# Kernel optimization log

Measured on AMD Instinct MI355X. Metric: run time of the kernel, lower is better.

## Reference

```python
import math
import jax, jax.numpy as jnp
import numpy as np

D_MODEL = 1024
D_STATE = 16
D_CONV = 4
EXPAND = 2
N_MOD = 2
D_INNER = EXPAND * D_MODEL
DT_RANK = math.ceil(D_MODEL / 16)
B_SZ = 2
SEQLEN = 2048


def setup_inputs() -> dict:
    key = jax.random.key(0)
    ks = jax.random.split(key, 10)
    hidden_states = jax.random.normal(ks[0], (B_SZ, SEQLEN, D_MODEL), jnp.float32)
    modality_ids = jax.random.randint(ks[1], (B_SZ, SEQLEN), 0, N_MOD).astype(jnp.int32)
    W_in = jax.random.normal(ks[2], (N_MOD, 2 * D_INNER, D_MODEL), jnp.float32) * (D_MODEL ** -0.5)
    conv_w = jax.random.normal(ks[3], (D_INNER, D_CONV), jnp.float32) * (D_CONV ** -0.5)
    conv_b = jnp.zeros((D_INNER,), jnp.float32)
    W_x = jax.random.normal(ks[4], (N_MOD, DT_RANK + 2 * D_STATE, D_INNER), jnp.float32) * (D_INNER ** -0.5)
    dt_init_std = DT_RANK ** -0.5
    W_dt = jax.random.uniform(ks[5], (N_MOD, D_INNER, DT_RANK), jnp.float32, -dt_init_std, dt_init_std)
    # dt bias init: inverse-softplus of dt ~ LogUniform(dt_min, dt_max), per Mamba
    dt = jnp.exp(jax.random.uniform(ks[6], (N_MOD, D_INNER), jnp.float32)
                 * (math.log(0.1) - math.log(0.001)) + math.log(0.001))
    dt = jnp.maximum(dt, 1e-4)
    b_dt = dt + jnp.log(-jnp.expm1(-dt))
    A_log = jnp.log(jnp.broadcast_to(jnp.arange(1, D_STATE + 1, dtype=jnp.float32), (D_INNER, D_STATE)))
    D = jnp.ones((D_INNER,), jnp.float32)
    W_out = jax.random.normal(ks[7], (N_MOD, D_MODEL, D_INNER), jnp.float32) * (D_INNER ** -0.5)
    return dict(hidden_states=hidden_states, modality_ids=modality_ids, W_in=W_in,
                conv_w=conv_w, conv_b=conv_b, W_x=W_x, W_dt=W_dt, b_dt=b_dt,
                A_log=A_log, D=D, W_out=W_out)


def _expert_apply(x, W, ids):
    # x: [T, d_in], W: [E, d_out, d_in], ids: [T] -> per-token expert output [T, d_out]
    all_out = jnp.einsum('td,eod->teo', x, W)
    return jnp.take_along_axis(all_out, ids[:, None, None], axis=1)[:, 0, :]


def _forward(hidden_states, modality_ids, W_in, conv_w, conv_b, W_x, W_dt, b_dt, A_log, D, W_out):
    Bsz, L, d_model = hidden_states.shape
    d_inner, d_state = A_log.shape
    dt_rank = W_dt.shape[2]
    d_conv = conv_w.shape[1]
    ids = modality_ids.reshape(-1)  # [T]

    # per-modality in_proj dispatch/combine
    xz = _expert_apply(hidden_states.reshape(-1, d_model), W_in, ids)  # [T, 2*d_inner]
    xz = xz.reshape(Bsz, L, 2 * d_inner).transpose(0, 2, 1)            # [B, 2*d_inner, L]
    x, z = jnp.split(xz, 2, axis=1)                                    # [B, d_inner, L] each

    # causal depthwise conv1d (pad left d_conv-1, truncate to L) + SiLU
    xp = jnp.pad(x, ((0, 0), (0, 0), (d_conv - 1, 0)))
    xc = conv_b[None, :, None]
    for k in range(d_conv):
        xc = xc + conv_w[None, :, k:k + 1] * xp[:, :, k:k + L]
    x = jax.nn.silu(xc)

    # per-modality x_proj -> (dt, B, C)
    xt = x.transpose(0, 2, 1).reshape(-1, d_inner)                     # [T, d_inner]
    x_dbl = _expert_apply(xt, W_x, ids)
    dt, Bm, Cm = jnp.split(x_dbl, [dt_rank, dt_rank + d_state], axis=-1)

    # per-modality dt_proj (with bias), then softplus (delta_softplus=True)
    dt = _expert_apply(dt, W_dt, ids) + b_dt[ids]                      # [T, d_inner]
    dt = jax.nn.softplus(dt)

    A = -jnp.exp(A_log)                                                # [d_inner, d_state]

    # selective scan over sequence (time-major)
    dts = dt.reshape(Bsz, L, d_inner).transpose(1, 0, 2)               # [L, B, d_inner]
    Bms = Bm.reshape(Bsz, L, d_state).transpose(1, 0, 2)               # [L, B, d_state]
    Cms = Cm.reshape(Bsz, L, d_state).transpose(1, 0, 2)               # [L, B, d_state]
    xs = x.transpose(2, 0, 1)                                          # [L, B, d_inner]

    def step(state, inp):
        x_t, dt_t, B_t, C_t = inp
        dA = jnp.exp(dt_t[..., None] * A)                              # [B, d_inner, d_state]
        state = state * dA + (dt_t * x_t)[..., None] * B_t[:, None, :]
        y_t = jnp.einsum('bdn,bn->bd', state, C_t)
        return state, y_t

    init = jnp.zeros((Bsz, d_inner, d_state), jnp.float32)
    _, ys = jax.lax.scan(step, init, (xs, dts, Bms, Cms))              # ys: [L, B, d_inner]

    y = ys.transpose(1, 0, 2)                                          # [B, L, d_inner]
    y = y + x.transpose(0, 2, 1) * D[None, None, :]                    # skip D*u
    y = y * jax.nn.silu(z.transpose(0, 2, 1))                          # z gate

    # per-modality out_proj
    out = _expert_apply(y.reshape(-1, d_inner), W_out, ids)
    return out.reshape(Bsz, L, d_model)


def reference(hidden_states, modality_ids, W_in, conv_w, conv_b, W_x, W_dt, b_dt, A_log, D, W_out):
    return _forward(hidden_states, modality_ids, W_in, conv_w, conv_b, W_x, W_dt, b_dt, A_log, D, W_out)
```

## Files before the change

### kernel.cpp

```cpp
#include <hip/hip_runtime.h>
#include <hip/hip_bf16.h>
#include <math.h>

#define B_SZ 2
#define SEQLEN 2048
#define D_MODEL 1024
#define D_INNER 2048
#define D_STATE 16
#define D_CONV 4
#define DT_RANK 64
#define NTOK (B_SZ * SEQLEN)
#define XDBL 96
#define NC 32
#define LC 64
#define PADTOT (17 * 256)

typedef float f32x4 __attribute__((ext_vector_type(4)));
typedef unsigned int u32x4 __attribute__((ext_vector_type(4)));
typedef __hip_bfloat16 bf16;

__device__ __forceinline__ float siluf(float v) { return v / (1.f + __expf(-v)); }
__device__ __forceinline__ float softplusf(float v) {
  return (v > 20.f) ? v : __logf(1.f + __expf(v));
}

__device__ __forceinline__ void mfma_bf16(f32x4& acc, u32x4 a, u32x4 b) {
  asm volatile("v_mfma_f32_16x16x32_bf16 %0, %1, %2, %0" : "+v"(acc) : "v"(a), "v"(b));
}

__device__ __forceinline__ void gload16(const bf16* g, bf16* l) {
  __builtin_amdgcn_global_load_lds(
      (const __attribute__((address_space(1))) unsigned int*)g,
      (__attribute__((address_space(3))) unsigned int*)l, 16, 0, 0);
}

__global__ __launch_bounds__(1024) void k_perm(const int* __restrict__ ids, int* __restrict__ perm) {
  __shared__ int sc[1024];
  const int tid = threadIdx.x;
  int loc[4];
  int cnt = 0;
#pragma unroll
  for (int q = 0; q < 4; q++) {
    loc[q] = ids[tid * 4 + q];
    cnt += (loc[q] == 0);
  }
  sc[tid] = cnt;
  __syncthreads();
  for (int off = 1; off < 1024; off <<= 1) {
    int v = sc[tid];
    int u = (tid >= off) ? sc[tid - off] : 0;
    __syncthreads();
    sc[tid] = v + u;
    __syncthreads();
  }
  const int N0 = sc[1023];
  const int m0 = (N0 + 255) & ~255;
  const int N1 = NTOK - N0;
  for (int idx = tid; idx < PADTOT; idx += 1024)
    if ((idx >= N0 && idx < m0) || idx >= m0 + N1) perm[idx] = -1;
  int zb = sc[tid] - cnt;
#pragma unroll
  for (int q = 0; q < 4; q++) {
    int t = tid * 4 + q;
    if (loc[q] == 0) { perm[zb] = t; zb++; }
    else             { perm[m0 + (t - zb)] = t; }
  }
}

#define CVT_H   (NTOK * D_MODEL)
#define CVT_WIN (2 * 2 * D_INNER * D_MODEL)
#define CVT_WX  (2 * XDBL * D_INNER)
#define CVT_WDT (2 * D_INNER * DT_RANK)
#define CVT_WO  (2 * D_MODEL * D_INNER)
#define CVT_TOT (CVT_H + CVT_WIN + CVT_WX + CVT_WDT + CVT_WO)
__global__ __launch_bounds__(256) void k_cvtall(const float* __restrict__ h,
                                                const float* __restrict__ Win,
                                                const float* __restrict__ Wx,
                                                const float* __restrict__ Wdt,
                                                const float* __restrict__ Wout,
                                                bf16* __restrict__ hB, bf16* __restrict__ WinB,
                                                bf16* __restrict__ WxB, bf16* __restrict__ WdtB,
                                                bf16* __restrict__ WoB) {
  size_t i = ((size_t)blockIdx.x * 256 + threadIdx.x) * 8;
  const float* src; bf16* dst; size_t off;
  if (i < CVT_H)                          { src = h;    dst = hB;   off = i; }
  else if (i < CVT_H + CVT_WIN)           { src = Win;  dst = WinB; off = i - CVT_H; }
  else if (i < CVT_H + CVT_WIN + CVT_WX)  { src = Wx;   dst = WxB;  off = i - CVT_H - CVT_WIN; }
  else if (i < CVT_TOT - CVT_WO)          { src = Wdt;  dst = WdtB; off = i - CVT_H - CVT_WIN - CVT_WX; }
  else                                    { src = Wout; dst = WoB;  off = i - (CVT_TOT - CVT_WO); }
  float4 f0 = *(const float4*)&src[off];
  float4 f1 = *(const float4*)&src[off + 4];
  __align__(16) bf16 tmp[8];
  tmp[0] = __float2bfloat16(f0.x); tmp[1] = __float2bfloat16(f0.y);
  tmp[2] = __float2bfloat16(f0.z); tmp[3] = __float2bfloat16(f0.w);
  tmp[4] = __float2bfloat16(f1.x); tmp[5] = __float2bfloat16(f1.y);
  tmp[6] = __float2bfloat16(f1.z); tmp[7] = __float2bfloat16(f1.w);
  *(u32x4*)&dst[off] = *(const u32x4*)tmp;
}

template <int KDIM, int NW, int KSPLIT, int EPI>
__device__ __forceinline__ void gemmP_body(const bf16* __restrict__ actB,
                                           const int* __restrict__ perm,
                                           const int* __restrict__ ids,
                                           const bf16* __restrict__ WB,
                                           bf16* __restrict__ outx,
                                           bf16* __restrict__ outz,
                                           float* __restrict__ out0) {
  constexpr int KLEN = KDIM / KSPLIT;
  constexpr int NT = KLEN / 64;
  constexpr int NCOL = (EPI == 1) ? (D_MODEL / 128) : 0;
  __shared__ bf16 As[3][256 * 64];
  __shared__ bf16 Ws[3][128 * 64];
  const int tid = threadIdx.x;

  const int gx = gridDim.x;
  const int nwg = gx * gridDim.y;
  const int fid = blockIdx.y * gx + blockIdx.x;
  const int q8 = nwg >> 3;
  const int swz = (fid & 7) * q8 + (fid >> 3);
  const int bx = swz % gx, by = swz / gx;
  const int ot = (KSPLIT > 1) ? (bx % NCOL) * 128 : bx * 128;
  const int kz = (KSPLIT > 1) ? bx / NCOL : 0;
  const int kbase = kz * KLEN;
  const int tt = by * 256;

  const int lane = tid & 63, w = tid >> 6;
  const int wr = w >> 1, wc = w & 1;
  const int lr = lane & 15, lg = lane >> 4;

  const int t00 = perm[tt];
  const int eu = (t00 >= 0) ? ids[t00] : 0;
  const size_t wexp = (size_t)eu * NW * KDIM;

  const int kswz = ((lane & 7) ^ ((lane >> 3) & 7)) * 8;
  size_t aBase[4]; int aLds[4];
  size_t bBase[2]; int bLds[2];
#pragma unroll
  for (int v = 0; v < 4; v++) {
    const int row = w * 32 + v * 8 + (lane >> 3);
    int ta = perm[tt + row]; if (ta < 0) ta = 0;
    aBase[v] = (size_t)ta * KDIM + kswz;
    aLds[v] = (w * 32 + v * 8) * 64;
  }
#pragma unroll
  for (int v = 0; v < 2; v++) {
    const int row = w * 16 + v * 8 + (lane >> 3);
    bBase[v] = wexp + (size_t)(ot + row) * KDIM + kswz;
    bLds[v] = (w * 16 + v * 8) * 64;
  }

  f32x4 acc[4][4];
#pragma unroll
  for (int i = 0; i < 4; i++)
#pragma unroll
    for (int j = 0; j < 4; j++) acc[i][j] = (f32x4){0.f, 0.f, 0.f, 0.f};

#pragma unroll
  for (int kt = 0; kt < 2; kt++) {
    const int k0 = kbase + kt * 64;
    gload16(&actB[aBase[0] + k0], &As[kt][aLds[0]]);
    gload16(&actB[aBase[1] + k0], &As[kt][aLds[1]]);
    gload16(&actB[aBase[2] + k0], &As[kt][aLds[2]]);
    gload16(&actB[aBase[3] + k0], &As[kt][aLds[3]]);
    gload16(&WB[bBase[0] + k0], &Ws[kt][bLds[0]]);
    gload16(&WB[bBase[1] + k0], &Ws[kt][bLds[1]]);
  }

  int bR = 0, bS = 2;
  for (int kt = 0; kt < NT; ++kt) {
    const int kp = kbase + (kt + 2) * 64;
    const bool st = (kt + 2 < NT);
    if (st) {
      gload16(&actB[aBase[0] + kp], &As[bS][aLds[0]]);
      gload16(&actB[aBase[1] + kp], &As[bS][aLds[1]]);
      gload16(&WB[bBase[0] + kp], &Ws[bS][bLds[0]]);
    }
    if (kt < NT - 2)       asm volatile("s_waitcnt vmcnt(9)" ::: "memory");
    else if (kt == NT - 2) asm volatile("s_waitcnt vmcnt(6)" ::: "memory");
    else                   asm volatile("s_waitcnt vmcnt(0)" ::: "memory");
    asm volatile("s_barrier" ::: "memory");

    const bf16* Ab = As[bR];
    const bf16* Wb = Ws[bR];
    u32x4 a[4][2], b0[2][2];
#pragma unroll
    for (int f = 0; f < 4; f++)
#pragma unroll
      for (int s = 0; s < 2; s++) {
        const int row = wr * 64 + f * 16 + lr;
        a[f][s] = *(const u32x4*)&Ab[row * 64 + ((s * 4 + lg) ^ (row & 7)) * 8];
      }
#pragma unroll
    for (int j = 0; j < 2; j++)
#pragma unroll
      for (int s = 0; s < 2; s++) {
        const int row = wc * 64 + j * 16 + lr;
        b0[j][s] = *(const u32x4*)&Wb[row * 64 + ((s * 4 + lg) ^ (row & 7)) * 8];
      }
    __builtin_amdgcn_s_setprio(1);
#pragma unroll
    for (int f = 0; f < 4; f++)
#pragma unroll
      for (int j = 0; j < 2; j++) {
        mfma_bf16(acc[f][j], a[f][0], b0[j][0]);
        mfma_bf16(acc[f][j], a[f][1], b0[j][1]);
      }
    __builtin_amdgcn_s_setprio(0);

    if (st) {
      gload16(&actB[aBase[2] + kp], &As[bS][aLds[2]]);
      gload16(&actB[aBase[3] + kp], &As[bS][aLds[3]]);
      gload16(&WB[bBase[1] + kp], &Ws[bS][bLds[1]]);
    }
    u32x4 b1[2][2];
#pragma unroll
    for (int j = 0; j < 2; j++)
#pragma unroll
      for (int s = 0; s < 2; s++) {
        const int row = wc * 64 + (2 + j) * 16 + lr;
        b1[j][s] = *(const u32x4*)&Wb[row * 64 + ((s * 4 + lg) ^ (row & 7)) * 8];
      }
    __builtin_amdgcn_s_setprio(1);
#pragma unroll
    for (int f = 0; f < 4; f++)
#pragma unroll
      for (int j = 0; j < 2; j++) {
        mfma_bf16(acc[f][2 + j], a[f][0], b1[j][0]);
        mfma_bf16(acc[f][2 + j], a[f][1], b1[j][1]);
      }
    __builtin_amdgcn_s_setprio(0);
    asm volatile("s_waitcnt lgkmcnt(0)" ::: "memory");
    asm volatile("s_barrier" ::: "memory");
    bR = (bR == 2) ? 0 : bR + 1;
    bS = (bS == 2) ? 0 : bS + 1;
  }

#pragma unroll
  for (int i = 0; i < 4; i++) {
#pragma unroll
    for (int r = 0; r < 4; r++) {
      const int m = wr * 64 + i * 16 + lg * 4 + r;
      const int t = perm[tt + m];
      if (t < 0) continue;
#pragma unroll
      for (int j = 0; j < 4; j++) {
        const int col = ot + wc * 64 + j * 16 + lr;
        const float v = acc[i][j][r];
        if (EPI == 0) {
          const bf16 vb = __float2bfloat16(v);
          if (col < D_INNER) outx[(size_t)t * D_INNER + col] = vb;
          else outz[(size_t)t * D_INNER + (col - D_INNER)] = vb;
        } else {
          out0[((size_t)kz * NTOK + t) * D_MODEL + col] = v;
        }
      }
    }
  }
}

__global__ __launch_bounds__(512) void k_inproj(const bf16* actB, const int* perm, const int* ids,
                                                const bf16* WB, bf16* outx, bf16* outz) {
  gemmP_body<D_MODEL, 2 * D_INNER, 1, 0>(actB, perm, ids, WB, outx, outz, nullptr);
}
__global__ __launch_bounds__(512) void k_outproj(const bf16* actB, const int* perm, const int* ids,
                                                 const bf16* WB, float* out0) {
  gemmP_body<D_INNER, D_MODEL, 2, 1>(actB, perm, ids, WB, nullptr, nullptr, out0);
}

__global__ __launch_bounds__(256) void k_xdblg(const bf16* __restrict__ actB,
                                               const int* __restrict__ perm,
                                               const int* __restrict__ ids,
                                               const bf16* __restrict__ WB,
                                               float* __restrict__ out0) {
  constexpr int KDIM = D_INNER, NW = XDBL, LDO = XDBL, KSPLIT = 8;
  constexpr int KLEN = KDIM / KSPLIT;
  __shared__ bf16 As[128 * 64];
  __shared__ bf16 Ws[128 * 64];
  __shared__ int permL[128];
  const int tid = threadIdx.x;
  const int bx = blockIdx.x, by = blockIdx.y;

  const int ot = 0;
  const int kz = bx;
  const int kbase = kz * KLEN;
  const int tt = by * 128;

  if (tid < 128) permL[tid] = perm[tt + tid];

  const int lane = tid & 63, w = tid >> 6;
  const int wr = w >> 1, wc = w & 1;
  const int lr = lane & 15, lg = lane >> 4;

  const int t00 = perm[tt];
  const int eu = (t00 >= 0) ? ids[t00] : 0;
  const size_t wexp = (size_t)eu * NW * KDIM;

  const int srow = w * 32 + (lane >> 3);
  const int scol = (lane & 7) * 8;
  size_t abase[4], bbase[4];
  int ldsoff[4];
#pragma unroll
  for (int v = 0; v < 4; v++) {
    const int row = srow + v * 8;
    int ta = perm[tt + row];
    if (ta < 0) ta = 0;
    abase[v] = (size_t)ta * KDIM + scol;
    int orow = ot + row;
    orow = (orow < NW) ? orow : (NW - 1);
    bbase[v] = wexp + (size_t)orow * KDIM + scol;
    ldsoff[v] = (w * 32 + v * 8) * 64;
  }

  f32x4 acc[4][4];
#pragma unroll
  for (int i = 0; i < 4; i++)
#pragma unroll
    for (int j = 0; j < 4; j++) acc[i][j] = (f32x4){0.f, 0.f, 0.f, 0.f};

  for (int k0 = kbase; k0 < kbase + KLEN; k0 += 64) {
#pragma unroll
    for (int v = 0; v < 4; v++) {
      gload16(&actB[abase[v] + k0], &As[ldsoff[v]]);
      gload16(&WB[bbase[v] + k0], &Ws[ldsoff[v]]);
    }
    __syncthreads();
#pragma unroll
    for (int ks = 0; ks < 64; ks += 32) {
      u32x4 a[4], b[4];
#pragma unroll
      for (int f = 0; f < 4; f++)
        a[f] = *(const u32x4*)&As[(wr * 64 + f * 16 + lr) * 64 + ks + lg * 8];
#pragma unroll
      for (int f = 0; f < 4; f++)
        b[f] = *(const u32x4*)&Ws[(wc * 64 + f * 16 + lr) * 64 + ks + lg * 8];
#pragma unroll
      for (int i = 0; i < 4; i++)
#pragma unroll
        for (int j = 0; j < 4; j++) mfma_bf16(acc[i][j], a[i], b[j]);
    }
    __syncthreads();
  }

#pragma unroll
  for (int i = 0; i < 4; i++) {
#pragma unroll
    for (int r = 0; r < 4; r++) {
      const int m = wr * 64 + i * 16 + lg * 4 + r;
      const int t = permL[m];
      if (t < 0) continue;
#pragma unroll
      for (int j = 0; j < 4; j++) {
        const int col = ot + wc * 64 + j * 16 + lr;
        if (col < NW) out0[((size_t)kz * NTOK + t) * LDO + col] = acc[i][j][r];
      }
    }
  }
}

__global__ __launch_bounds__(256, 4) void k_dtv(const float* __restrict__ xdbl,
                                                const int* __restrict__ perm,
                                                const int* __restrict__ ids,
                                                const float* __restrict__ Wdt,
                                                const float* __restrict__ bdt,
                                                bf16* __restrict__ dtB) {
  __shared__ float Xs[64][65];
  __shared__ float Ws[64][65];
  __shared__ int permL[64];
  const int tid = threadIdx.x;
  const int tt = blockIdx.y * 64;
  const int cb = blockIdx.x * 64;
  if (tid < 64) permL[tid] = perm[tt + tid];
  const int t0 = perm[tt];
  const int e = (t0 >= 0) ? ids[t0] : 0;
  {
    const int r = tid >> 2, q = (tid & 3) * 16;
    int ta = perm[tt + r];
    if (ta < 0) ta = 0;
    const float* xsrc = &xdbl[(size_t)ta * XDBL + q];
    const float* wsrc = &Wdt[((size_t)e * D_INNER + cb + r) * DT_RANK + q];
#pragma unroll
    for (int u = 0; u < 4; u++) {
      float4 xv = *(const float4*)&xsrc[u * 4];
      float4 wv = *(const float4*)&wsrc[u * 4];
      *(float4*)&Xs[r][q + u * 4] = xv;
      *(float4*)&Ws[r][q + u * 4] = wv;
    }
  }
  __syncthreads();
  const int tl = (tid & 15) * 4;
  const int cl = (tid >> 4) * 4;
  float acc[4][4] = {};
#pragma unroll 2
  for (int k4 = 0; k4 < 16; k4++) {
    float4 xv[4], wv[4];
#pragma unroll
    for (int i = 0; i < 4; i++) xv[i] = *(const float4*)&Xs[tl + i][k4 * 4];
#pragma unroll
    for (int j = 0; j < 4; j++) wv[j] = *(const float4*)&Ws[cl + j][k4 * 4];
#pragma unroll
    for (int i = 0; i < 4; i++)
#pragma unroll
      for (int j = 0; j < 4; j++) {
        acc[i][j] = fmaf(xv[i].x, wv[j].x, acc[i][j]);
        acc[i][j] = fmaf(xv[i].y, wv[j].y, acc[i][j]);
        acc[i][j] = fmaf(xv[i].z, wv[j].z, acc[i][j]);
        acc[i][j] = fmaf(xv[i].w, wv[j].w, acc[i][j]);
      }
  }
#pragma unroll
  for (int i = 0; i < 4; i++) {
    const int t = permL[tl + i];
    if (t < 0) continue;
    __align__(8) bf16 ov[4];
#pragma unroll
    for (int j = 0; j < 4; j++)
      ov[j] = __float2bfloat16(softplusf(acc[i][j] + bdt[e * D_INNER + cb + cl + j]));
    *(uint2*)&dtB[(size_t)t * D_INNER + cb + cl] = *(const uint2*)ov;
  }
}

__global__ __launch_bounds__(256) void k_xred(const float* __restrict__ part,
                                              float* __restrict__ xdbl) {
  const int i = blockIdx.x * 256 + threadIdx.x;
  float s = 0.f;
#pragma unroll
  for (int k = 0; k < 8; k++) s += part[(size_t)k * NTOK * XDBL + i];
  xdbl[i] = s;
}

__global__ __launch_bounds__(256) void k_ored2(const float* __restrict__ part,
                                               float* __restrict__ out) {
  const size_t base = ((size_t)blockIdx.x * 256 + threadIdx.x) * 4;
  constexpr size_t NM = (size_t)NTOK * D_MODEL;
  float4 s = *(const float4*)&part[base];
  float4 p = *(const float4*)&part[NM + base];
  s.x += p.x; s.y += p.y; s.z += p.z; s.w += p.w;
  *(float4*)&out[base] = s;
}

__global__ __launch_bounds__(256) void k_conv(const bf16* __restrict__ xrawB,
                                              const float* __restrict__ cw,
                                              const float* __restrict__ cb,
                                              bf16* __restrict__ xB) {
  int idx = blockIdx.x * 256 + threadIdx.x;
  int c = idx & (D_INNER - 1);
  int t = idx >> 11;
  int l = t & (SEQLEN - 1);
  int b = t >> 11;
  float acc = cb[c];
#pragma unroll
  for (int k = 0; k < D_CONV; k++) {
    int ll = l + k - (D_CONV - 1);
    if (ll >= 0)
      acc = fmaf(cw[c * D_CONV + k],
                 __bfloat162float(xrawB[((size_t)(b * SEQLEN + ll)) * D_INNER + c]), acc);
  }
  xB[(size_t)idx] = __float2bfloat16(siluf(acc));
}

__global__ __launch_bounds__(256) void k_scan_part(const bf16* __restrict__ xB,
                                                   const bf16* __restrict__ dtB,
                                                   const float* __restrict__ xdbl,
                                                   const float* __restrict__ A_log,
                                                   float* __restrict__ F,
                                                   float* __restrict__ Sdt) {
  __shared__ float Bs[LC][D_STATE];
  const int tid = threadIdx.x;
  const int j = blockIdx.y;
  const int ch = blockIdx.x * 256 + tid;
  const int b = ch >> 11, c = ch & (D_INNER - 1);
  const int t0 = (b << 11) + j * LC;
  {
    int l = tid >> 2, q = (tid & 3) * 4;
    *(float4*)&Bs[l][q] = *(const float4*)&xdbl[(size_t)(t0 + l) * XDBL + DT_RANK + q];
  }
  float Ar[D_STATE];
#pragma unroll
  for (int n4 = 0; n4 < 4; n4++) {
    float4 a = *(const float4*)&A_log[(size_t)c * D_STATE + n4 * 4];
    Ar[n4 * 4 + 0] = -__expf(a.x); Ar[n4 * 4 + 1] = -__expf(a.y);
    Ar[n4 * 4 + 2] = -__expf(a.z); Ar[n4 * 4 + 3] = -__expf(a.w);
  }
  __syncthreads();
  float st[D_STATE];
#pragma unroll
  for (int n = 0; n < D_STATE; n++) st[n] = 0.f;
  float sdt = 0.f;
  float dtc = __bfloat162float(dtB[(size_t)t0 * D_INNER + c]);
  float xc = __bfloat162float(xB[(size_t)t0 * D_INNER + c]);
  for (int l = 0; l < LC; l++) {
    float dtn = 0.f, xn = 0.f;
    if (l < LC - 1) {
      dtn = __bfloat162float(dtB[(size_t)(t0 + l + 1) * D_INNER + c]);
      xn = __bfloat162float(xB[(size_t)(t0 + l + 1) * D_INNER + c]);
    }
    const float dtx = dtc * xc;
    sdt += dtc;
#pragma unroll
    for (int n = 0; n < D_STATE; n++) {
      float dA = __expf(dtc * Ar[n]);
      st[n] = fmaf(st[n], dA, dtx * Bs[l][n]);
    }
    dtc = dtn; xc = xn;
  }
  const size_t fb = ((size_t)j * NTOK + ch) * D_STATE;
#pragma unroll
  for (int n4 = 0; n4 < 4; n4++)
    *(float4*)&F[fb + n4 * 4] = make_float4(st[n4 * 4], st[n4 * 4 + 1], st[n4 * 4 + 2], st[n4 * 4 + 3]);
  Sdt[(size_t)j * NTOK + ch] = sdt;
}

__global__ __launch_bounds__(256) void k_combine(const float* __restrict__ F,
                                                 const float* __restrict__ Sdt,
                                                 const float* __restrict__ A_log,
                                                 float* __restrict__ s0) {
  const int gid = blockIdx.x * 256 + threadIdx.x;
  const int ch = gid >> 4, n = gid & 15, c = ch & (D_INNER - 1);
  const float Ar = -__expf(A_log[(size_t)c * D_STATE + n]);
  float s = 0.f;
  for (int j = 0; j < NC; j++) {
    s0[((size_t)j * NTOK + ch) * D_STATE + n] = s;
    s = fmaf(s, __expf(Ar * Sdt[(size_t)j * NTOK + ch]), F[((size_t)j * NTOK + ch) * D_STATE + n]);
  }
}

__global__ __launch_bounds__(256) void k_scan_fin(const bf16* __restrict__ xB,
                                                  const bf16* __restrict__ dtB,
                                                  const float* __restrict__ xdbl,
                                                  const bf16* __restrict__ zB,
                                                  const float* __restrict__ A_log,
                                                  const float* __restrict__ Dp,
                                                  const float* __restrict__ s0,
                                                  bf16* __restrict__ ybuf) {
  __shared__ float Bs[LC][D_STATE];
  __shared__ float Cs[LC][D_STATE];
  const int tid = threadIdx.x;
  const int j = blockIdx.y;
  const int ch = blockIdx.x * 256 + tid;
  const int b = ch >> 11, c = ch & (D_INNER - 1);
  const int t0 = (b << 11) + j * LC;
  {
    int l = tid >> 2, q = (tid & 3) * 4;
    *(float4*)&Bs[l][q] = *(const float4*)&xdbl[(size_t)(t0 + l) * XDBL + DT_RANK + q];
    *(float4*)&Cs[l][q] = *(const float4*)&xdbl[(size_t)(t0 + l) * XDBL + DT_RANK + D_STATE + q];
  }
  float Ar[D_STATE];
#pragma unroll
  for (int n4 = 0; n4 < 4; n4++) {
    float4 a = *(const float4*)&A_log[(size_t)c * D_STATE + n4 * 4];
    Ar[n4 * 4 + 0] = -__expf(a.x); Ar[n4 * 4 + 1] = -__expf(a.y);
    Ar[n4 * 4 + 2] = -__expf(a.z); Ar[n4 * 4 + 3] = -__expf(a.w);
  }
  __syncthreads();
  float st[D_STATE];
  const size_t sb = ((size_t)j * NTOK + ch) * D_STATE;
#pragma unroll
  for (int n4 = 0; n4 < 4; n4++) {
    float4 s = *(const float4*)&s0[sb + n4 * 4];
    st[n4 * 4 + 0] = s.x; st[n4 * 4 + 1] = s.y; st[n4 * 4 + 2] = s.z; st[n4 * 4 + 3] = s.w;
  }
  const float Dc = Dp[c];
  float dtc = __bfloat162float(dtB[(size_t)t0 * D_INNER + c]);
  float xc = __bfloat162float(xB[(size_t)t0 * D_INNER + c]);
  for (int l = 0; l < LC; l++) {
    float dtn = 0.f, xn = 0.f;
    if (l < LC - 1) {
      dtn = __bfloat162float(dtB[(size_t)(t0 + l + 1) * D_INNER + c]);
      xn = __bfloat162float(xB[(size_t)(t0 + l + 1) * D_INNER + c]);
    }
    const float zv = __bfloat162float(zB[(size_t)(t0 + l) * D_INNER + c]);
    const float dtx = dtc * xc;
    float y = 0.f;
#pragma unroll
    for (int n = 0; n < D_STATE; n++) {
      float dA = __expf(dtc * Ar[n]);
      st[n] = fmaf(st[n], dA, dtx * Bs[l][n]);
      y = fmaf(st[n], Cs[l][n], y);
    }
    float yv = fmaf(xc, Dc, y);
    ybuf[(size_t)(t0 + l) * D_INNER + c] = __float2bfloat16(yv * siluf(zv));
    dtc = dtn; xc = xn;
  }
}

extern "C" void kernel_launch(void* const* d_in, const int* in_sizes, int n_in,
                              void* d_out, int out_size, void* d_ws, size_t ws_size,
                              hipStream_t stream) {
  const float* h = (const float*)d_in[0];
  const int* ids = (const int*)d_in[1];
  const float* Win = (const float*)d_in[2];
  const float* cw = (const float*)d_in[3];
  const float* cb = (const float*)d_in[4];
  const float* Wx = (const float*)d_in[5];
  const float* Wdt = (const float*)d_in[6];
  const float* bdt = (const float*)d_in[7];
  const float* Alog = (const float*)d_in[8];
  const float* Dp = (const float*)d_in[9];
  const float* Wout = (const float*)d_in[10];
  float* out = (float*)d_out;

  const size_t NTD = (size_t)NTOK * D_INNER;
  float* ws = (float*)d_ws;
  float* slot0 = ws + 0 * NTD;
  float* slot1 = ws + 1 * NTD;
  float* slot2 = ws + 2 * NTD;
  float* slot3 = ws + 3 * NTD;
  size_t cur = 4 * NTD;
  float* xdbl_p = ws + cur; cur += (size_t)NTOK * XDBL;
  float* sdt_p = ws + cur; cur += (size_t)NC * NTOK;
  int* perm = (int*)(ws + cur); cur += PADTOT;
  bf16* xB = (bf16*)(ws + cur); cur += NTD / 2;
  bf16* WoB = (bf16*)(ws + cur); cur += CVT_WO / 2;
  bf16* WxB = (bf16*)(ws + cur); cur += CVT_WX / 2;
  bf16* WdtB = (bf16*)(ws + cur); cur += CVT_WDT / 2;

  bf16* hB = (bf16*)slot0;
  bf16* dtbB = (bf16*)slot0;
  bf16* zB = (bf16*)slot1;
  bf16* WinB = (bf16*)slot2;
  float* part = slot2;
  float* part2 = slot1;
  bf16* xrawB = (bf16*)slot3;
  float* F = slot3;
  bf16* yB = (bf16*)slot3;
  float* s0 = (float*)d_out;

  k_perm<<<1, 1024, 0, stream>>>(ids, perm);
  k_cvtall<<<CVT_TOT / 8 / 256, 256, 0, stream>>>(h, Win, Wx, Wdt, Wout, hB, WinB, WxB, WdtB, WoB);
  k_inproj<<<dim3(32, 17), 512, 0, stream>>>(hB, perm, ids, WinB, xrawB, zB);
  k_conv<<<NTD / 256, 256, 0, stream>>>(xrawB, cw, cb, xB);
  k_xdblg<<<dim3(8, 34), 256, 0, stream>>>(xB, perm, ids, WxB, part);
  k_xred<<<NTOK * XDBL / 256, 256, 0, stream>>>(part, xdbl_p);
  k_dtv<<<dim3(32, PADTOT / 64), 256, 0, stream>>>(xdbl_p, perm, ids, Wdt, bdt, dtbB);
  k_scan_part<<<dim3(16, NC), 256, 0, stream>>>(xB, dtbB, xdbl_p, Alog, F, sdt_p);
  k_combine<<<256, 256, 0, stream>>>(F, sdt_p, Alog, s0);
  k_scan_fin<<<dim3(16, NC), 256, 0, stream>>>(xB, dtbB, xdbl_p, zB, Alog, Dp, s0, yB);
  k_outproj<<<dim3(16, 17), 512, 0, stream>>>(yB, perm, ids, WoB, part2);
  k_ored2<<<NTOK * D_MODEL / 4 / 256, 256, 0, stream>>>(part2, out);
}
```

Measured before the change: 321.6 us.

## Use 256x256 double-buffered GEMM tiles and store scan chunk states in bf16

The grouped GEMM body changes from a 256x128 triple-buffered tile to a 256x256 double-buffered tile with 8x4 MFMA fragments per wave. This halves the in_proj and out_proj grids and improves operand reuse per LDS load. Separately, the per-chunk scan states F and the combined initial states s0 are now stored in bf16 instead of fp32, which halves their memory traffic. The costs are fewer workgroups, higher register pressure, shallower prefetch, and lower precision in the scan carry states.

```diff
diff --git a/kernel.cpp b/kernel.cpp
--- a/kernel.cpp
+++ b/kernel.cpp
@@ -99,7 +99,7 @@
 }
 
 template <int KDIM, int NW, int KSPLIT, int EPI>
-__device__ __forceinline__ void gemmP_body(const bf16* __restrict__ actB,
+__device__ __forceinline__ void gemmQ_body(const bf16* __restrict__ actB,
                                            const int* __restrict__ perm,
                                            const int* __restrict__ ids,
                                            const bf16* __restrict__ WB,
@@ -108,9 +108,9 @@
                                            float* __restrict__ out0) {
   constexpr int KLEN = KDIM / KSPLIT;
   constexpr int NT = KLEN / 64;
-  constexpr int NCOL = (EPI == 1) ? (D_MODEL / 128) : 0;
-  __shared__ bf16 As[3][256 * 64];
-  __shared__ bf16 Ws[3][128 * 64];
+  constexpr int NCOL = NW / 256;
+  __shared__ bf16 As[2][256 * 64];
+  __shared__ bf16 Ws[2][256 * 64];
   const int tid = threadIdx.x;
 
   const int gx = gridDim.x;
@@ -119,127 +119,89 @@
   const int q8 = nwg >> 3;
   const int swz = (fid & 7) * q8 + (fid >> 3);
   const int bx = swz % gx, by = swz / gx;
-  const int ot = (KSPLIT > 1) ? (bx % NCOL) * 128 : bx * 128;
+  const int ot = (KSPLIT > 1) ? (bx % NCOL) * 256 : bx * 256;
   const int kz = (KSPLIT > 1) ? bx / NCOL : 0;
   const int kbase = kz * KLEN;
   const int tt = by * 256;
 
   const int lane = tid & 63, w = tid >> 6;
-  const int wr = w >> 1, wc = w & 1;
+  const int wr = w >> 2, wc = w & 3;
   const int lr = lane & 15, lg = lane >> 4;
 
   const int t00 = perm[tt];
   const int eu = (t00 >= 0) ? ids[t00] : 0;
   const size_t wexp = (size_t)eu * NW * KDIM;
 
-  const int kswz = ((lane & 7) ^ ((lane >> 3) & 7)) * 8;
-  size_t aBase[4]; int aLds[4];
-  size_t bBase[2]; int bLds[2];
+  const int srow_l = lane >> 3;
+  const int kswz = ((lane & 7) ^ srow_l) * 8;
+  size_t aBase[4], bBase[4];
+  int ldsE[4];
 #pragma unroll
   for (int v = 0; v < 4; v++) {
-    const int row = w * 32 + v * 8 + (lane >> 3);
-    int ta = perm[tt + row]; if (ta < 0) ta = 0;
+    const int row = (w * 4 + v) * 8 + srow_l;
+    int ta = perm[tt + row];
+    if (ta < 0) ta = 0;
     aBase[v] = (size_t)ta * KDIM + kswz;
-    aLds[v] = (w * 32 + v * 8) * 64;
-  }
-#pragma unroll
-  for (int v = 0; v < 2; v++) {
-    const int row = w * 16 + v * 8 + (lane >> 3);
     bBase[v] = wexp + (size_t)(ot + row) * KDIM + kswz;
-    bLds[v] = (w * 16 + v * 8) * 64;
-  }
-
-  f32x4 acc[4][4];
-#pragma unroll
-  for (int i = 0; i < 4; i++)
+    ldsE[v] = (w * 4 + v) * 512;
+  }
+
+  f32x4 acc[8][4];
+#pragma unroll
+  for (int i = 0; i < 8; i++)
 #pragma unroll
     for (int j = 0; j < 4; j++) acc[i][j] = (f32x4){0.f, 0.f, 0.f, 0.f};
 
-#pragma unroll
-  for (int kt = 0; kt < 2; kt++) {
-    const int k0 = kbase + kt * 64;
-    gload16(&actB[aBase[0] + k0], &As[kt][aLds[0]]);
-    gload16(&actB[aBase[1] + k0], &As[kt][aLds[1]]);
-    gload16(&actB[aBase[2] + k0], &As[kt][aLds[2]]);
-    gload16(&actB[aBase[3] + k0], &As[kt][aLds[3]]);
-    gload16(&WB[bBase[0] + k0], &Ws[kt][bLds[0]]);
-    gload16(&WB[bBase[1] + k0], &Ws[kt][bLds[1]]);
-  }
-
-  int bR = 0, bS = 2;
+  auto STAGE = [&](int buf, int k0) {
+#pragma unroll
+    for (int v = 0; v < 4; v++) {
+      gload16(&actB[aBase[v] + k0], &As[buf][ldsE[v]]);
+      gload16(&WB[bBase[v] + k0], &Ws[buf][ldsE[v]]);
+    }
+  };
+
+  STAGE(0, kbase);
+  int cur = 0;
   for (int kt = 0; kt < NT; ++kt) {
-    const int kp = kbase + (kt + 2) * 64;
-    const bool st = (kt + 2 < NT);
-    if (st) {
-      gload16(&actB[aBase[0] + kp], &As[bS][aLds[0]]);
-      gload16(&actB[aBase[1] + kp], &As[bS][aLds[1]]);
-      gload16(&WB[bBase[0] + kp], &Ws[bS][bLds[0]]);
-    }
-    if (kt < NT - 2)       asm volatile("s_waitcnt vmcnt(9)" ::: "memory");
-    else if (kt == NT - 2) asm volatile("s_waitcnt vmcnt(6)" ::: "memory");
-    else                   asm volatile("s_waitcnt vmcnt(0)" ::: "memory");
+    if (kt + 1 < NT) {
+      STAGE(cur ^ 1, kbase + (kt + 1) * 64);
+      asm volatile("s_waitcnt vmcnt(8)" ::: "memory");
+    } else {
+      asm volatile("s_waitcnt vmcnt(0)" ::: "memory");
+    }
     asm volatile("s_barrier" ::: "memory");
-
-    const bf16* Ab = As[bR];
-    const bf16* Wb = Ws[bR];
-    u32x4 a[4][2], b0[2][2];
-#pragma unroll
-    for (int f = 0; f < 4; f++)
-#pragma unroll
-      for (int s = 0; s < 2; s++) {
-        const int row = wr * 64 + f * 16 + lr;
-        a[f][s] = *(const u32x4*)&Ab[row * 64 + ((s * 4 + lg) ^ (row & 7)) * 8];
+    const bf16* Ab = As[cur];
+    const bf16* Wb = Ws[cur];
+#pragma unroll
+    for (int s = 0; s < 2; s++) {
+      u32x4 a[8], b[4];
+#pragma unroll
+      for (int f = 0; f < 8; f++) {
+        const int row = wr * 128 + f * 16 + lr;
+        a[f] = *(const u32x4*)&Ab[row * 64 + ((s * 4 + lg) ^ (row & 7)) * 8];
       }
 #pragma unroll
-    for (int j = 0; j < 2; j++)
-#pragma unroll
-      for (int s = 0; s < 2; s++) {
+      for (int j = 0; j < 4; j++) {
         const int row = wc * 64 + j * 16 + lr;
-        b0[j][s] = *(const u32x4*)&Wb[row * 64 + ((s * 4 + lg) ^ (row & 7)) * 8];
+        b[j] = *(const u32x4*)&Wb[row * 64 + ((s * 4 + lg) ^ (row & 7)) * 8];
       }
-    __builtin_amdgcn_s_setprio(1);
-#pragma unroll
-    for (int f = 0; f < 4; f++)
-#pragma unroll
-      for (int j = 0; j < 2; j++) {
-        mfma_bf16(acc[f][j], a[f][0], b0[j][0]);
-        mfma_bf16(acc[f][j], a[f][1], b0[j][1]);
-      }
-    __builtin_amdgcn_s_setprio(0);
-
-    if (st) {
-      gload16(&actB[aBase[2] + kp], &As[bS][aLds[2]]);
-      gload16(&actB[aBase[3] + kp], &As[bS][aLds[3]]);
-      gload16(&WB[bBase[1] + kp], &Ws[bS][bLds[1]]);
-    }
-    u32x4 b1[2][2];
-#pragma unroll
-    for (int j = 0; j < 2; j++)
-#pragma unroll
-      for (int s = 0; s < 2; s++) {
-        const int row = wc * 64 + (2 + j) * 16 + lr;
-        b1[j][s] = *(const u32x4*)&Wb[row * 64 + ((s * 4 + lg) ^ (row & 7)) * 8];
-      }
-    __builtin_amdgcn_s_setprio(1);
-#pragma unroll
-    for (int f = 0; f < 4; f++)
-#pragma unroll
-      for (int j = 0; j < 2; j++) {
-        mfma_bf16(acc[f][2 + j], a[f][0], b1[j][0]);
-        mfma_bf16(acc[f][2 + j], a[f][1], b1[j][1]);
-      }
-    __builtin_amdgcn_s_setprio(0);
+      __builtin_amdgcn_s_setprio(1);
+#pragma unroll
+      for (int f = 0; f < 8; f++)
+#pragma unroll
+        for (int j = 0; j < 4; j++) mfma_bf16(acc[f][j], a[f], b[j]);
+      __builtin_amdgcn_s_setprio(0);
+    }
     asm volatile("s_waitcnt lgkmcnt(0)" ::: "memory");
     asm volatile("s_barrier" ::: "memory");
-    bR = (bR == 2) ? 0 : bR + 1;
-    bS = (bS == 2) ? 0 : bS + 1;
-  }
-
-#pragma unroll
-  for (int i = 0; i < 4; i++) {
+    cur ^= 1;
+  }
+
+#pragma unroll
+  for (int i = 0; i < 8; i++) {
 #pragma unroll
     for (int r = 0; r < 4; r++) {
-      const int m = wr * 64 + i * 16 + lg * 4 + r;
+      const int m = wr * 128 + i * 16 + lg * 4 + r;
       const int t = perm[tt + m];
       if (t < 0) continue;
 #pragma unroll
@@ -260,11 +222,11 @@
 
 __global__ __launch_bounds__(512) void k_inproj(const bf16* actB, const int* perm, const int* ids,
                                                 const bf16* WB, bf16* outx, bf16* outz) {
-  gemmP_body<D_MODEL, 2 * D_INNER, 1, 0>(actB, perm, ids, WB, outx, outz, nullptr);
+  gemmQ_body<D_MODEL, 2 * D_INNER, 1, 0>(actB, perm, ids, WB, outx, outz, nullptr);
 }
 __global__ __launch_bounds__(512) void k_outproj(const bf16* actB, const int* perm, const int* ids,
                                                  const bf16* WB, float* out0) {
-  gemmP_body<D_INNER, D_MODEL, 2, 1>(actB, perm, ids, WB, nullptr, nullptr, out0);
+  gemmQ_body<D_INNER, D_MODEL, 2, 1>(actB, perm, ids, WB, nullptr, nullptr, out0);
 }
 
 __global__ __launch_bounds__(256) void k_xdblg(const bf16* __restrict__ actB,
@@ -462,7 +424,7 @@
                                                    const bf16* __restrict__ dtB,
                                                    const float* __restrict__ xdbl,
                                                    const float* __restrict__ A_log,
-                                                   float* __restrict__ F,
+                                                   bf16* __restrict__ F,
                                                    float* __restrict__ Sdt) {
   __shared__ float Bs[LC][D_STATE];
   const int tid = threadIdx.x;
@@ -504,23 +466,26 @@
     dtc = dtn; xc = xn;
   }
   const size_t fb = ((size_t)j * NTOK + ch) * D_STATE;
-#pragma unroll
-  for (int n4 = 0; n4 < 4; n4++)
-    *(float4*)&F[fb + n4 * 4] = make_float4(st[n4 * 4], st[n4 * 4 + 1], st[n4 * 4 + 2], st[n4 * 4 + 3]);
+  __align__(16) bf16 fv[16];
+#pragma unroll
+  for (int n = 0; n < D_STATE; n++) fv[n] = __float2bfloat16(st[n]);
+  *(u32x4*)&F[fb] = *(const u32x4*)fv;
+  *(u32x4*)&F[fb + 8] = *(const u32x4*)(fv + 8);
   Sdt[(size_t)j * NTOK + ch] = sdt;
 }
 
-__global__ __launch_bounds__(256) void k_combine(const float* __restrict__ F,
+__global__ __launch_bounds__(256) void k_combine(const bf16* __restrict__ F,
                                                  const float* __restrict__ Sdt,
                                                  const float* __restrict__ A_log,
-                                                 float* __restrict__ s0) {
+                                                 bf16* __restrict__ s0) {
   const int gid = blockIdx.x * 256 + threadIdx.x;
   const int ch = gid >> 4, n = gid & 15, c = ch & (D_INNER - 1);
   const float Ar = -__expf(A_log[(size_t)c * D_STATE + n]);
   float s = 0.f;
   for (int j = 0; j < NC; j++) {
-    s0[((size_t)j * NTOK + ch) * D_STATE + n] = s;
-    s = fmaf(s, __expf(Ar * Sdt[(size_t)j * NTOK + ch]), F[((size_t)j * NTOK + ch) * D_STATE + n]);
+    s0[((size_t)j * NTOK + ch) * D_STATE + n] = __float2bfloat16(s);
+    s = fmaf(s, __expf(Ar * Sdt[(size_t)j * NTOK + ch]),
+             __bfloat162float(F[((size_t)j * NTOK + ch) * D_STATE + n]));
   }
 }
 
@@ -530,7 +495,7 @@
                                                   const bf16* __restrict__ zB,
                                                   const float* __restrict__ A_log,
                                                   const float* __restrict__ Dp,
-                                                  const float* __restrict__ s0,
+                                                  const bf16* __restrict__ s0,
                                                   bf16* __restrict__ ybuf) {
   __shared__ float Bs[LC][D_STATE];
   __shared__ float Cs[LC][D_STATE];
@@ -555,10 +520,7 @@
   float st[D_STATE];
   const size_t sb = ((size_t)j * NTOK + ch) * D_STATE;
 #pragma unroll
-  for (int n4 = 0; n4 < 4; n4++) {
-    float4 s = *(const float4*)&s0[sb + n4 * 4];
-    st[n4 * 4 + 0] = s.x; st[n4 * 4 + 1] = s.y; st[n4 * 4 + 2] = s.z; st[n4 * 4 + 3] = s.w;
-  }
+  for (int n = 0; n < D_STATE; n++) st[n] = __bfloat162float(s0[sb + n]);
   const float Dc = Dp[c];
   float dtc = __bfloat162float(dtB[(size_t)t0 * D_INNER + c]);
   float xc = __bfloat162float(xB[(size_t)t0 * D_INNER + c]);
@@ -621,13 +583,13 @@
   float* part = slot2;
   float* part2 = slot1;
   bf16* xrawB = (bf16*)slot3;
-  float* F = slot3;
+  bf16* F = (bf16*)slot3;
   bf16* yB = (bf16*)slot3;
-  float* s0 = (float*)d_out;
+  bf16* s0 = (bf16*)d_out;
 
   k_perm<<<1, 1024, 0, stream>>>(ids, perm);
   k_cvtall<<<CVT_TOT / 8 / 256, 256, 0, stream>>>(h, Win, Wx, Wdt, Wout, hB, WinB, WxB, WdtB, WoB);
-  k_inproj<<<dim3(32, 17), 512, 0, stream>>>(hB, perm, ids, WinB, xrawB, zB);
+  k_inproj<<<dim3(16, 17), 512, 0, stream>>>(hB, perm, ids, WinB, xrawB, zB);
   k_conv<<<NTD / 256, 256, 0, stream>>>(xrawB, cw, cb, xB);
   k_xdblg<<<dim3(8, 34), 256, 0, stream>>>(xB, perm, ids, WxB, part);
   k_xred<<<NTOK * XDBL / 256, 256, 0, stream>>>(part, xdbl_p);
@@ -635,6 +597,6 @@
   k_scan_part<<<dim3(16, NC), 256, 0, stream>>>(xB, dtbB, xdbl_p, Alog, F, sdt_p);
   k_combine<<<256, 256, 0, stream>>>(F, sdt_p, Alog, s0);
   k_scan_fin<<<dim3(16, NC), 256, 0, stream>>>(xB, dtbB, xdbl_p, zB, Alog, Dp, s0, yB);
-  k_outproj<<<dim3(16, 17), 512, 0, stream>>>(yB, perm, ids, WoB, part2);
+  k_outproj<<<dim3(8, 17), 512, 0, stream>>>(yB, perm, ids, WoB, part2);
   k_ored2<<<NTOK * D_MODEL / 4 / 256, 256, 0, stream>>>(part2, out);
 }
```

New measurement: 303.1 us. 1.06x faster.
